# Kernel optimization log

Hardware: AMD Instinct MI355X
Metric: run time of the kernel (lower is better)

The kernel has to match this reference:

```python
import jax, jax.numpy as jnp
import numpy as np

B, S, H, V = 4, 2048, 768, 32000
HID = 100          # self.hidden_size
N_LABELS = 3
LN2 = 0.6931471805599453


def setup_inputs() -> dict:
    key = jax.random.key(0)
    ks = jax.random.split(key, 10)
    return {
        "input_ids": jax.random.randint(ks[0], (B, S), 0, V),
        "attention_mask": jnp.ones((B, S), jnp.float32),
        "sentiment": jax.random.normal(ks[1], (B, 3), jnp.float32),
        "hidden_states": jax.random.normal(ks[2], (B, S, H), jnp.float32),
        "lm_logits": jax.random.normal(ks[3], (B, S, V), jnp.float32),
        "W_ih": jax.random.normal(ks[4], (4 * HID, H + 1), jnp.float32) * 0.05,
        "W_hh": jax.random.normal(ks[5], (4 * HID, HID), jnp.float32) * 0.05,
        "b_ih": jax.random.normal(ks[6], (4 * HID,), jnp.float32) * 0.05,
        "b_hh": jax.random.normal(ks[7], (4 * HID,), jnp.float32) * 0.05,
        "cls_W": jax.random.normal(ks[8], (N_LABELS, HID + 3), jnp.float32) * 0.05,
        "cls_b": jax.random.normal(ks[9], (N_LABELS,), jnp.float32) * 0.05,
    }


def _lstm_last(x, W_ih, W_hh, b_ih, b_hh):
    # x: [B,S,D] -> last hidden state [B,HID]; PyTorch gate order i,f,g,o
    b, hid = x.shape[0], W_hh.shape[1]
    x_proj = jnp.einsum('bsd,gd->bsg', x, W_ih) + b_ih + b_hh  # [B,S,4H]

    def step(carry, xt):
        h, c = carry
        gates = xt + h @ W_hh.T
        i, f, g, o = jnp.split(gates, 4, axis=-1)
        c = jax.nn.sigmoid(f) * c + jax.nn.sigmoid(i) * jnp.tanh(g)
        h = jax.nn.sigmoid(o) * jnp.tanh(c)
        return (h, c), None

    h0 = jnp.zeros((b, hid), x.dtype)
    (hT, _), _ = jax.lax.scan(step, (h0, h0), jnp.swapaxes(x_proj, 0, 1))
    return hT


def reference(input_ids, attention_mask, sentiment, hidden_states, lm_logits,
              W_ih, W_hh, b_ih, b_hh, cls_W, cls_b):
    # surprisal: -log2(softmax(logits)[input_ids]) * mask, detached
    log_p = jax.nn.log_softmax(lm_logits, axis=-1)                       # [B,S,V]
    lp = jnp.take_along_axis(log_p, input_ids[..., None], axis=2)[..., 0]  # [B,S]
    surp = jax.lax.stop_gradient((-lp / LN2) * attention_mask)

    x = jnp.concatenate([hidden_states, surp[..., None]], axis=-1)  # [B,S,H+1]
    hT = _lstm_last(x, W_ih, W_hh, b_ih, b_hh)                      # [B,HID]
    # dropout is identity at inference
    feat = jnp.concatenate([hT, sentiment], axis=1)                 # [B,HID+3]
    return feat @ cls_W.T + cls_b                                   # [B,N_LABELS]
```

## Files before the change

### kernel.cpp

```cpp
#include <hip/hip_runtime.h>
#include <hip/hip_bf16.h>
#include <math.h>

#define B 4
#define S 2048
#define H 768
#define V 32000
#define HID 100
#define G4 400
#define M_TOT (B*S)

typedef _Float16 half2_t __attribute__((ext_vector_type(2)));
typedef _Float16 half8_t __attribute__((ext_vector_type(8)));

__device__ __forceinline__ float fdot2_(half2_t a, half2_t b, float c) {
#if __has_builtin(__builtin_amdgcn_fdot2)
  return __builtin_amdgcn_fdot2(a, b, c, false);
#else
  return c + (float)a[0] * (float)b[0] + (float)a[1] * (float)b[1];
#endif
}

__device__ __forceinline__ float sigmoidf_(float x) {
  return 1.0f / (1.0f + __expf(-x));
}
__device__ __forceinline__ float tanhf_(float x) {
  float ax = fabsf(x);
  float e = __expf(-2.0f * ax);
  float t = (1.0f - e) / (1.0f + e);
  return copysignf(t, x);
}

__global__ __launch_bounds__(256) void surprisal_kernel(
    const float* __restrict__ logits, const int* __restrict__ ids,
    const float* __restrict__ mask, float* __restrict__ surp) {
  int row = blockIdx.x;
  const float* x = logits + (size_t)row * V;
  int tid = threadIdx.x;
  float m = -INFINITY, s = 0.0f;
  const float4* x4 = (const float4*)x;
  for (int i = tid; i < V / 4; i += 256) {
    float4 v = x4[i];
    float mv = fmaxf(fmaxf(v.x, v.y), fmaxf(v.z, v.w));
    if (mv > m) { s *= __expf(m - mv); m = mv; }
    s += __expf(v.x - m) + __expf(v.y - m) + __expf(v.z - m) + __expf(v.w - m);
  }
  #pragma unroll
  for (int off = 32; off > 0; off >>= 1) {
    float mo = __shfl_xor(m, off);
    float so = __shfl_xor(s, off);
    float mn = fmaxf(m, mo);
    s = s * __expf(m - mn) + so * __expf(mo - mn);
    m = mn;
  }
  __shared__ float sm[4], ss[4];
  int wid = tid >> 6, lane = tid & 63;
  if (lane == 0) { sm[wid] = m; ss[wid] = s; }
  __syncthreads();
  if (tid == 0) {
    float M = sm[0], Ssum = ss[0];
    #pragma unroll
    for (int w = 1; w < 4; ++w) {
      float mo = sm[w], so = ss[w];
      float mn = fmaxf(M, mo);
      Ssum = Ssum * __expf(M - mn) + so * __expf(mo - mn);
      M = mn;
    }
    float xid = x[ids[row]];
    surp[row] = (M + __logf(Ssum) - xid) * 1.4426950408889634f * mask[row];
  }
}

#define BM 64
#define BN 64
#define BK 32

__global__ __launch_bounds__(256) void xproj_kernel(
    const float* __restrict__ A,
    const float* __restrict__ surp,
    const float* __restrict__ W,
    const float* __restrict__ b_ih, const float* __restrict__ b_hh,
    float* __restrict__ xproj) {
  __shared__ float As[BK][BM];
  __shared__ float Bs[BK][BN];
  int tid = threadIdx.x;
  int m0 = blockIdx.x * BM;
  int n0 = blockIdx.y * BN;
  int tx = tid & 15, ty = tid >> 4;
  float acc[4][4] = {};
  for (int k0 = 0; k0 < H; k0 += BK) {
    #pragma unroll
    for (int l = 0; l < 2; ++l) {
      int idx = tid + l * 256;
      int row = idx >> 3;
      int kq = idx & 7;
      float4 v = *(const float4*)&A[(size_t)(m0 + row) * H + k0 + kq * 4];
      As[kq * 4 + 0][row] = v.x;
      As[kq * 4 + 1][row] = v.y;
      As[kq * 4 + 2][row] = v.z;
      As[kq * 4 + 3][row] = v.w;
    }
    #pragma unroll
    for (int l = 0; l < 8; ++l) {
      int idx = tid + l * 256;
      int n = idx >> 5;
      int kk = idx & 31;
      int gn = n0 + n;
      Bs[kk][n] = (gn < G4) ? W[(size_t)gn * (H + 1) + k0 + kk] : 0.0f;
    }
    __syncthreads();
    #pragma unroll
    for (int k = 0; k < BK; ++k) {
      float4 a = *(const float4*)&As[k][ty * 4];
      float4 bq = *(const float4*)&Bs[k][tx * 4];
      float av[4] = {a.x, a.y, a.z, a.w};
      float bv[4] = {bq.x, bq.y, bq.z, bq.w};
      #pragma unroll
      for (int i = 0; i < 4; ++i)
        #pragma unroll
        for (int j = 0; j < 4; ++j)
          acc[i][j] += av[i] * bv[j];
    }
    __syncthreads();
  }
  #pragma unroll
  for (int i = 0; i < 4; ++i) {
    int gm = m0 + ty * 4 + i;
    float sv = surp[gm];
    #pragma unroll
    for (int j = 0; j < 4; ++j) {
      int gn = n0 + tx * 4 + j;
      if (gn < G4) {
        float val = acc[i][j] + sv * W[(size_t)gn * (H + 1) + H] + b_ih[gn] + b_hh[gn];
        xproj[(size_t)gm * G4 + gn] = val;
      }
    }
  }
}

#define NH2 52
__global__ __launch_bounds__(256, 1) void lstm_kernel(
    const float* __restrict__ xproj,
    const float* __restrict__ W_hh,
    const float* __restrict__ sent,
    const float* __restrict__ cls_W,
    const float* __restrict__ cls_b,
    float* __restrict__ out) {
  int b = blockIdx.x;
  int tid = threadIdx.x;
  __shared__ __align__(16) _Float16 h_s[2 * NH2];
  __shared__ float gates_s[G4];

  half2_t w0[NH2], w1[NH2];
  int r0 = 2 * tid, r1 = 2 * tid + 1;
  if (tid < 200) {
    const float* wr0 = W_hh + (size_t)r0 * HID;
    const float* wr1 = W_hh + (size_t)r1 * HID;
    #pragma unroll
    for (int j = 0; j < 50; ++j) {
      w0[j] = half2_t{(_Float16)wr0[2 * j], (_Float16)wr0[2 * j + 1]};
      w1[j] = half2_t{(_Float16)wr1[2 * j], (_Float16)wr1[2 * j + 1]};
    }
    #pragma unroll
    for (int j = 50; j < NH2; ++j) { w0[j] = half2_t{0, 0}; w1[j] = half2_t{0, 0}; }
  }
  float c_reg = 0.0f;
  if (tid < 2 * NH2) h_s[tid] = (_Float16)0;
  __syncthreads();

  const float* xp = xproj + (size_t)b * S * G4;
  float2 xv = (tid < 200) ? ((const float2*)xp)[tid] : float2{0.f, 0.f};

  for (int t = 0; t < S; ++t) {
    int tn = (t + 1 < S) ? (t + 1) : t;
    float2 xv_next = (tid < 200) ? ((const float2*)(xp + (size_t)tn * G4))[tid]
                                 : float2{0.f, 0.f};

    if (tid < 200) {
      float a0 = 0.f, a1 = 0.f;
      const half8_t* h8 = (const half8_t*)h_s;
      #pragma unroll
      for (int j = 0; j < 13; ++j) {
        half8_t hv = h8[j];
        half2_t ha = {hv[0], hv[1]}, hb = {hv[2], hv[3]};
        half2_t hc = {hv[4], hv[5]}, hd = {hv[6], hv[7]};
        a0 = fdot2_(w0[4 * j + 0], ha, a0);
        a1 = fdot2_(w1[4 * j + 0], ha, a1);
        a0 = fdot2_(w0[4 * j + 1], hb, a0);
        a1 = fdot2_(w1[4 * j + 1], hb, a1);
        a0 = fdot2_(w0[4 * j + 2], hc, a0);
        a1 = fdot2_(w1[4 * j + 2], hc, a1);
        a0 = fdot2_(w0[4 * j + 3], hd, a0);
        a1 = fdot2_(w1[4 * j + 3], hd, a1);
      }
      *(float2*)&gates_s[r0] = float2{a0 + xv.x, a1 + xv.y};
    }
    __syncthreads();
    if (tid < HID) {
      float ig = sigmoidf_(gates_s[tid]);
      float fg = sigmoidf_(gates_s[HID + tid]);
      float gg = tanhf_(gates_s[2 * HID + tid]);
      float og = sigmoidf_(gates_s[3 * HID + tid]);
      c_reg = fg * c_reg + ig * gg;
      h_s[tid] = (_Float16)(og * tanhf_(c_reg));
    }
    xv = xv_next;
    __syncthreads();
  }

  if (tid < 3) {
    float acc = cls_b[tid];
    const float* cw = cls_W + tid * (HID + 3);
    #pragma unroll
    for (int j = 0; j < HID; ++j) acc += cw[j] * (float)h_s[j];
    #pragma unroll
    for (int k2 = 0; k2 < 3; ++k2) acc += cw[HID + k2] * sent[b * 3 + k2];
    out[b * 3 + tid] = acc;
  }
}

extern "C" void kernel_launch(void* const* d_in, const int* in_sizes, int n_in,
                              void* d_out, int out_size, void* d_ws, size_t ws_size,
                              hipStream_t stream) {
  const int*   input_ids = (const int*)d_in[0];
  const float* mask      = (const float*)d_in[1];
  const float* sent      = (const float*)d_in[2];
  const float* hs        = (const float*)d_in[3];
  const float* logits    = (const float*)d_in[4];
  const float* W_ih      = (const float*)d_in[5];
  const float* W_hh      = (const float*)d_in[6];
  const float* b_ih      = (const float*)d_in[7];
  const float* b_hh      = (const float*)d_in[8];
  const float* cls_W     = (const float*)d_in[9];
  const float* cls_b     = (const float*)d_in[10];
  float* out = (float*)d_out;

  float* surp  = (float*)d_ws;
  float* xproj = surp + M_TOT;

  surprisal_kernel<<<M_TOT, 256, 0, stream>>>(logits, input_ids, mask, surp);
  xproj_kernel<<<dim3(M_TOT / BM, (G4 + BN - 1) / BN), 256, 0, stream>>>(
      hs, surp, W_ih, b_ih, b_hh, xproj);
  lstm_kernel<<<B, 256, 0, stream>>>(xproj, W_hh, sent, cls_W, cls_b, out);
}
```

Before: 1.706 ms.

## Restructure LSTM step with gate-interleaved rows, shuffles, and double-buffered h

Assigns each thread-pair the i/f and g/o gate rows for one hidden unit, so the gate nonlinearities are computed in parallel and exchanged through lane shuffles instead of a shared gates buffer. This removes one of the two block barriers per timestep. The hidden state is now double-buffered in shared memory, and xproj values are prefetched PD steps ahead in a register ring. tanh is rewritten in terms of sigmoid, and the dot product is split into two accumulators per row to shorten the dependency chain. In exchange, the loads of xproj become scalar and strided, and the slot indexing into the register array is dynamic, which may spill unless unrolling resolves it.

Result: slower. 2.040 ms (+19.5%).

```diff
diff --git a/kernel.cpp b/kernel.cpp
--- a/kernel.cpp
+++ b/kernel.cpp
@@ -9,6 +9,7 @@
 #define HID 100
 #define G4 400
 #define M_TOT (B*S)
+#define PD 4
 
 typedef _Float16 half2_t __attribute__((ext_vector_type(2)));
 typedef _Float16 half8_t __attribute__((ext_vector_type(8)));
@@ -24,11 +25,8 @@
 __device__ __forceinline__ float sigmoidf_(float x) {
   return 1.0f / (1.0f + __expf(-x));
 }
-__device__ __forceinline__ float tanhf_(float x) {
-  float ax = fabsf(x);
-  float e = __expf(-2.0f * ax);
-  float t = (1.0f - e) / (1.0f + e);
-  return copysignf(t, x);
+__device__ __forceinline__ float tanh_via_sig_(float x) {
+  return 2.0f * sigmoidf_(2.0f * x) - 1.0f;
 }
 
 __global__ __launch_bounds__(256) void surprisal_kernel(
@@ -148,63 +146,80 @@
     float* __restrict__ out) {
   int b = blockIdx.x;
   int tid = threadIdx.x;
-  __shared__ __align__(16) _Float16 h_s[2 * NH2];
-  __shared__ float gates_s[G4];
-
-  half2_t w0[NH2], w1[NH2];
-  int r0 = 2 * tid, r1 = 2 * tid + 1;
-  if (tid < 200) {
-    const float* wr0 = W_hh + (size_t)r0 * HID;
-    const float* wr1 = W_hh + (size_t)r1 * HID;
+  __shared__ __align__(16) _Float16 hb0[2 * NH2];
+  __shared__ __align__(16) _Float16 hb1[2 * NH2];
+
+  int k = tid >> 1;
+  int odd = tid & 1;
+  bool active = tid < 200;
+  int ra = odd ? (100 + k) : k;
+  int rb = odd ? (300 + k) : (200 + k);
+
+  half2_t wa[NH2], wb[NH2];
+  if (active) {
+    const float* pa = W_hh + (size_t)ra * HID;
+    const float* pb = W_hh + (size_t)rb * HID;
     #pragma unroll
     for (int j = 0; j < 50; ++j) {
-      w0[j] = half2_t{(_Float16)wr0[2 * j], (_Float16)wr0[2 * j + 1]};
-      w1[j] = half2_t{(_Float16)wr1[2 * j], (_Float16)wr1[2 * j + 1]};
-    }
-    #pragma unroll
-    for (int j = 50; j < NH2; ++j) { w0[j] = half2_t{0, 0}; w1[j] = half2_t{0, 0}; }
-  }
+      wa[j] = half2_t{(_Float16)pa[2 * j], (_Float16)pa[2 * j + 1]};
+      wb[j] = half2_t{(_Float16)pb[2 * j], (_Float16)pb[2 * j + 1]};
+    }
+  }
+  #pragma unroll
+  for (int j = 50; j < NH2; ++j) { wa[j] = half2_t{0, 0}; wb[j] = half2_t{0, 0}; }
+
   float c_reg = 0.0f;
-  if (tid < 2 * NH2) h_s[tid] = (_Float16)0;
+  if (tid < 2 * NH2) { hb0[tid] = (_Float16)0; hb1[tid] = (_Float16)0; }
   __syncthreads();
 
   const float* xp = xproj + (size_t)b * S * G4;
-  float2 xv = (tid < 200) ? ((const float2*)xp)[tid] : float2{0.f, 0.f};
-
+  float xa[PD], xb[PD];
+  #pragma unroll
+  for (int d = 0; d < PD; ++d) {
+    xa[d] = active ? xp[(size_t)d * G4 + ra] : 0.0f;
+    xb[d] = active ? xp[(size_t)d * G4 + rb] : 0.0f;
+  }
+
+  #pragma unroll 4
   for (int t = 0; t < S; ++t) {
-    int tn = (t + 1 < S) ? (t + 1) : t;
-    float2 xv_next = (tid < 200) ? ((const float2*)(xp + (size_t)tn * G4))[tid]
-                                 : float2{0.f, 0.f};
-
-    if (tid < 200) {
-      float a0 = 0.f, a1 = 0.f;
-      const half8_t* h8 = (const half8_t*)h_s;
-      #pragma unroll
-      for (int j = 0; j < 13; ++j) {
-        half8_t hv = h8[j];
-        half2_t ha = {hv[0], hv[1]}, hb = {hv[2], hv[3]};
-        half2_t hc = {hv[4], hv[5]}, hd = {hv[6], hv[7]};
-        a0 = fdot2_(w0[4 * j + 0], ha, a0);
-        a1 = fdot2_(w1[4 * j + 0], ha, a1);
-        a0 = fdot2_(w0[4 * j + 1], hb, a0);
-        a1 = fdot2_(w1[4 * j + 1], hb, a1);
-        a0 = fdot2_(w0[4 * j + 2], hc, a0);
-        a1 = fdot2_(w1[4 * j + 2], hc, a1);
-        a0 = fdot2_(w0[4 * j + 3], hd, a0);
-        a1 = fdot2_(w1[4 * j + 3], hd, a1);
-      }
-      *(float2*)&gates_s[r0] = float2{a0 + xv.x, a1 + xv.y};
-    }
-    __syncthreads();
-    if (tid < HID) {
-      float ig = sigmoidf_(gates_s[tid]);
-      float fg = sigmoidf_(gates_s[HID + tid]);
-      float gg = tanhf_(gates_s[2 * HID + tid]);
-      float og = sigmoidf_(gates_s[3 * HID + tid]);
-      c_reg = fg * c_reg + ig * gg;
-      h_s[tid] = (_Float16)(og * tanhf_(c_reg));
-    }
-    xv = xv_next;
+    int slot = t & (PD - 1);
+    const half8_t* hr = (t & 1) ? (const half8_t*)hb1 : (const half8_t*)hb0;
+    _Float16* hw = (t & 1) ? hb0 : hb1;
+
+    float a0 = 0.f, a1 = 0.f, b0 = 0.f, b1 = 0.f;
+    #pragma unroll
+    for (int j = 0; j < 13; ++j) {
+      half8_t hv = hr[j];
+      half2_t h0 = {hv[0], hv[1]}, h1 = {hv[2], hv[3]};
+      half2_t h2 = {hv[4], hv[5]}, h3 = {hv[6], hv[7]};
+      a0 = fdot2_(wa[4 * j + 0], h0, a0);
+      b0 = fdot2_(wb[4 * j + 0], h0, b0);
+      a1 = fdot2_(wa[4 * j + 1], h1, a1);
+      b1 = fdot2_(wb[4 * j + 1], h1, b1);
+      a0 = fdot2_(wa[4 * j + 2], h2, a0);
+      b0 = fdot2_(wb[4 * j + 2], h2, b0);
+      a1 = fdot2_(wa[4 * j + 3], h3, a1);
+      b1 = fdot2_(wb[4 * j + 3], h3, b1);
+    }
+    float ga = a0 + a1 + xa[slot];
+    float gb = b0 + b1 + xb[slot];
+
+    int tp = t + PD;
+    if (tp < S) {
+      xa[slot] = active ? xp[(size_t)tp * G4 + ra] : 0.0f;
+      xb[slot] = active ? xp[(size_t)tp * G4 + rb] : 0.0f;
+    }
+
+    float ta = sigmoidf_(ga);
+    float sb = sigmoidf_(odd ? gb : 2.0f * gb);
+    float tb = odd ? sb : (2.0f * sb - 1.0f);
+    float pa_ = __shfl_xor(ta, 1);
+    float pb_ = __shfl_xor(tb, 1);
+    if (active && !odd) {
+      c_reg = pa_ * c_reg + ta * tb;
+      float h = pb_ * tanh_via_sig_(c_reg);
+      hw[k] = (_Float16)h;
+    }
     __syncthreads();
   }
 
@@ -212,7 +227,7 @@
     float acc = cls_b[tid];
     const float* cw = cls_W + tid * (HID + 3);
     #pragma unroll
-    for (int j = 0; j < HID; ++j) acc += cw[j] * (float)h_s[j];
+    for (int j = 0; j < HID; ++j) acc += cw[j] * (float)hb0[j];
     #pragma unroll
     for (int k2 = 0; k2 < 3; ++k2) acc += cw[HID + k2] * sent[b * 3 + k2];
     out[b * 3 + tid] = acc;
```
